# Performance work log

Measured on AMD Instinct MI355X. Metric: run time of the kernel, lower is better.

The kernel has to match this reference:

```python
import jax, jax.numpy as jnp
import numpy as np

NUM_HEADS = 16
HEAD_DIM = 64
HIDDEN = NUM_HEADS * HEAD_DIM


def _rope_tables(seq_len, dim, dtype):
    # inv_freq: [dim/2]; emb = cat(freqs, freqs): [S, dim]
    inv_freq = 1.0 / (10000.0 ** (jnp.arange(0, dim, 2, dtype=jnp.float32) / dim))
    t = jnp.arange(seq_len, dtype=jnp.float32)
    freqs = jnp.einsum('i,j->ij', t, inv_freq)
    emb = jnp.concatenate([freqs, freqs], axis=-1)
    return jnp.cos(emb).astype(dtype), jnp.sin(emb).astype(dtype)  # [S, dim] each


def _rotate_half(x):
    x1, x2 = jnp.split(x, 2, axis=-1)
    return jnp.concatenate([-x2, x1], axis=-1)


def setup_inputs() -> dict:
    key = jax.random.key(0)
    k1, k2, k3, k4 = jax.random.split(key, 4)
    B, S = 2, 2048
    hidden_states = jax.random.normal(k1, (B, S, HIDDEN), dtype=jnp.float32)
    scale = 0.02
    Wq = jax.random.normal(k2, (HIDDEN, HIDDEN), dtype=jnp.float32) * scale
    Wk = jax.random.normal(k3, (HIDDEN, HIDDEN), dtype=jnp.float32) * scale
    Wv = jax.random.normal(k4, (HIDDEN, HIDDEN), dtype=jnp.float32) * scale
    return {"hidden_states": hidden_states, "Wq": Wq, "Wk": Wk, "Wv": Wv}


def reference(hidden_states, Wq, Wk, Wv):
    B, S, H = hidden_states.shape
    # nn.Linear: x @ W.T ; reshape to [B, heads, S, head_dim]
    def split_heads(x):
        return x.reshape(B, S, NUM_HEADS, HEAD_DIM).transpose(0, 2, 1, 3)
    q = split_heads(hidden_states @ Wq.T)
    k = split_heads(hidden_states @ Wk.T)
    v = split_heads(hidden_states @ Wv.T)
    # inline RoPE over full head_dim
    cos, sin = _rope_tables(S, HEAD_DIM, q.dtype)  # [S, head_dim]
    cos = cos[None, None]  # [1,1,S,head_dim]
    sin = sin[None, None]
    q = q * cos + _rotate_half(q) * sin
    k = k * cos + _rotate_half(k) * sin
    # manual softmax attention
    scores = jnp.einsum('bhqd,bhkd->bhqk', q, k) / (HEAD_DIM ** 0.5)
    probs = jax.nn.softmax(scores, axis=-1)
    ctx = jnp.einsum('bhqk,bhkd->bhqd', probs, v)
    ctx = ctx.transpose(0, 2, 1, 3).reshape(B, S, H)
    return ctx
```

## Files before the change

### kernel.cpp

```cpp
#include <hip/hip_runtime.h>
#include <math.h>

#define NHEADS 16
#define HDIM   64
#define HID    1024
#define BATCH  2
#define SEQ    2048
#define NX (BATCH*SEQ*HID)
#define NW (HID*HID)

typedef unsigned short u16;
typedef __attribute__((ext_vector_type(8))) short  bf16x8;
typedef __attribute__((ext_vector_type(8))) unsigned short u16x8;
typedef __attribute__((ext_vector_type(4))) float  f32x4;


__device__ __forceinline__ void split8(const float* xf, bf16x8& hi, bf16x8& lo) {
#pragma unroll
    for (int j = 0; j < 8; j++) {
        unsigned u = __float_as_uint(xf[j]);
        hi[j] = (short)(u >> 16);
        float hf = __uint_as_float(u & 0xFFFF0000u);
        lo[j] = (short)(__float_as_uint(xf[j] - hf) >> 16);
    }
}
__device__ __forceinline__ void split1(float v, u16& h, u16& l) {
    unsigned u = __float_as_uint(v);
    h = (u16)(u >> 16);
    l = (u16)(__float_as_uint(v - __uint_as_float(u & 0xFFFF0000u)) >> 16);
}

__global__ void rope_tables_kernel(float* __restrict__ ct, float* __restrict__ st) {
    int idx = blockIdx.x * 256 + threadIdx.x;
    if (idx >= SEQ * HDIM) return;
    int s  = idx >> 6;
    int dh = idx & 63;
    int i  = dh & 31;
    float inv = exp2f(-(float)i * (13.28771237954945f / 32.0f));
    float fr  = (float)s * inv;
    ct[idx] = cosf(fr);
    st[idx] = sinf(fr);
}

__global__ void split_kernel(const float* __restrict__ X,
                             const float* __restrict__ W0,
                             const float* __restrict__ W1,
                             const float* __restrict__ W2,
                             u16* __restrict__ Xhi, u16* __restrict__ Xlo,
                             u16* __restrict__ Whi, u16* __restrict__ Wlo)
{
    long idx = ((long)blockIdx.x * 256 + threadIdx.x) * 4;
    if (idx >= (long)NX + 3L * NW) return;
    const float* src; u16* dh; u16* dl; long off;
    if (idx < NX) { src = X; dh = Xhi; dl = Xlo; off = idx; }
    else {
        long rr = idx - NX;
        int wi = (int)(rr >> 20);
        off = rr & (NW - 1);
        src = (wi == 0) ? W0 : ((wi == 1) ? W1 : W2);
        dh = Whi + (size_t)wi * NW;
        dl = Wlo + (size_t)wi * NW;
    }
    const int r = (int)(off >> 10);
    const int k = (int)(off & 1023);
    const size_t fo = ((size_t)(r >> 4) * 32 + (k >> 5)) * 512
                    + (size_t)((k >> 3) & 3) * 128 + (size_t)(r & 15) * 8 + (k & 7);
    float4 v = *(const float4*)(src + off);
    const float* vf = (const float*)&v;
    ushort4 h4, l4;
    u16* hp = (u16*)&h4; u16* lp = (u16*)&l4;
#pragma unroll
    for (int e = 0; e < 4; e++) split1(vf[e], hp[e], lp[e]);
    *(ushort4*)(dh + fo) = h4;
    *(ushort4*)(dl + fo) = l4;
}

__global__ __launch_bounds__(256, 2) void qkv_mfma_kernel(
    const u16* __restrict__ Xhi, const u16* __restrict__ Xlo,
    const u16* __restrict__ Whi, const u16* __restrict__ Wlo,
    const float* __restrict__ ct, const float* __restrict__ st,
    u16* __restrict__ Qhi, u16* __restrict__ Qlo,
    u16* __restrict__ Khi, u16* __restrict__ Klo,
    u16* __restrict__ Vhi, u16* __restrict__ Vlo)
{
    __shared__ unsigned vtr[64][129];

    const int t    = threadIdx.x;
    const int lane = t & 63;
    const int w    = t >> 6;
    const int lx   = lane & 15;
    const int quad = lane >> 4;
    const int proj = blockIdx.z;
    const int n0   = blockIdx.x * 128;
    const int m0   = blockIdx.y * 128;

    const u16* __restrict__ Wph = Whi + (size_t)proj * NW;
    const u16* __restrict__ Wpl = Wlo + (size_t)proj * NW;

    const int am = (w & 1) * 64;
    const int bn = (w >> 1) * 64;
    const int lp = quad * 128 + lx * 8;

    const u16 *pAh[4], *pAl[4], *pBh[4], *pBl[4];
#pragma unroll
    for (int i = 0; i < 4; i++) {
        const size_t o = ((size_t)(((m0 + am) >> 4) + i) * 32) * 512 + lp;
        pAh[i] = Xhi + o; pAl[i] = Xlo + o;
    }
#pragma unroll
    for (int j = 0; j < 4; j++) {
        const size_t o = ((size_t)(((n0 + bn) >> 4) + j) * 32) * 512 + lp;
        pBh[j] = Wph + o; pBl[j] = Wpl + o;
    }

    f32x4 acc[4][4];
#pragma unroll
    for (int i = 0; i < 4; i++)
#pragma unroll
        for (int j = 0; j < 4; j++) acc[i][j] = (f32x4){0.f, 0.f, 0.f, 0.f};

    bf16x8 cah[4], cal[4], cbh[4], cbl[4];
#pragma unroll
    for (int i = 0; i < 4; i++) { cah[i] = *(const bf16x8*)(pAh[i]); cal[i] = *(const bf16x8*)(pAl[i]); }
#pragma unroll
    for (int j = 0; j < 4; j++) { cbh[j] = *(const bf16x8*)(pBh[j]); cbl[j] = *(const bf16x8*)(pBl[j]); }

#pragma unroll 1
    for (int kt = 0; kt < HID; kt += 32) {
        const int ko = (kt + 32 < HID) ? ((kt + 32) >> 5) * 512 : 0;
        bf16x8 nah[4], nal[4], nbh[4], nbl[4];
#pragma unroll
        for (int i = 0; i < 4; i++) { nah[i] = *(const bf16x8*)(pAh[i] + ko); nal[i] = *(const bf16x8*)(pAl[i] + ko); }
#pragma unroll
        for (int j = 0; j < 4; j++) { nbh[j] = *(const bf16x8*)(pBh[j] + ko); nbl[j] = *(const bf16x8*)(pBl[j] + ko); }

#pragma unroll
        for (int j = 0; j < 4; j++)
#pragma unroll
            for (int i = 0; i < 4; i++) {
                acc[i][j] = __builtin_amdgcn_mfma_f32_16x16x32_bf16(cah[i], cbh[j], acc[i][j], 0, 0, 0);
                acc[i][j] = __builtin_amdgcn_mfma_f32_16x16x32_bf16(cal[i], cbh[j], acc[i][j], 0, 0, 0);
                acc[i][j] = __builtin_amdgcn_mfma_f32_16x16x32_bf16(cah[i], cbl[j], acc[i][j], 0, 0, 0);
            }
#pragma unroll
        for (int i = 0; i < 4; i++) { cah[i] = nah[i]; cal[i] = nal[i]; }
#pragma unroll
        for (int j = 0; j < 4; j++) { cbh[j] = nbh[j]; cbl[j] = nbl[j]; }
    }

    const int b      = m0 >> 11;
    const int head   = (n0 >> 6) + (w >> 1);
    const int m_base = m0 + am;

    if (proj < 2) {
#pragma unroll
        for (int i = 0; i < 4; i++) {
#pragma unroll
            for (int r = 0; r < 4; r++) {
                const int s = (m_base + i * 16 + quad * 4 + r) & 2047;
                const float* ctr = ct + s * HDIM;
                const float* str = st + s * HDIM;
                float nv[4];
#pragma unroll
                for (int j = 0; j < 4; j++) {
                    const int dh = j * 16 + lx;
                    const float c  = ctr[dh];
                    const float sn = str[dh];
                    const float x  = acc[i][j][r];
                    const float p  = acc[i][j ^ 2][r];
                    nv[j] = (j < 2) ? (x * c - p * sn) : (x * c + p * sn);
                }
#pragma unroll
                for (int j = 0; j < 4; j++) acc[i][j][r] = nv[j];
            }
        }
        u16* dh_ = (proj == 0) ? Qhi : Khi;
        u16* dl_ = (proj == 0) ? Qlo : Klo;
        const float qscale = (proj == 0) ? 0.18033688011112042f : 1.0f;
        const size_t obase = (size_t)(b * NHEADS + head) * SEQ * HDIM;
#pragma unroll
        for (int i = 0; i < 4; i++)
#pragma unroll
            for (int r = 0; r < 4; r++) {
                const int s   = (m_base + i * 16 + quad * 4 + r) & 2047;
                const int rb  = s >> 4;
                const int lxq = s & 15;
#pragma unroll
                for (int j = 0; j < 4; j++) {
                    const size_t fo = obase + ((size_t)rb * 2 + (j >> 1)) * 512
                                    + (size_t)((j & 1) * 2 + (lx >> 3)) * 128
                                    + (size_t)lxq * 8 + (lx & 7);
                    u16 hh, ll;
                    split1(acc[i][j][r] * qscale, hh, ll);
                    dh_[fo] = hh;
                    dl_[fo] = ll;
                }
            }
    } else {
#pragma unroll 1
        for (int pass = 0; pass < 2; pass++) {
            __syncthreads();
            if ((w & 1) == pass) {
#pragma unroll
                for (int i = 0; i < 4; i++)
#pragma unroll
                    for (int j = 0; j < 4; j++)
#pragma unroll
                        for (int r = 0; r < 4; r++) {
                            const int ml = i * 16 + quad * 4 + r;
                            const int nl = bn + j * 16 + lx;
                            const float v = acc[i][j][r];
                            unsigned u  = __float_as_uint(v);
                            unsigned hi = u & 0xFFFF0000u;
                            unsigned lo = __float_as_uint(v - __uint_as_float(hi)) >> 16;
                            vtr[ml][nl] = hi | lo;
                        }
            }
            __syncthreads();
            {
                const int d      = t >> 1;
                const int sh     = (t & 1) * 32;
                const int headv  = (n0 >> 6) + (d >> 6);
                const int dd     = d & 63;
                const size_t vbase = (size_t)(b * NHEADS + headv) * SEQ * HDIM;
                const int s0base = (m0 & 2047) + pass * 64 + sh;
#pragma unroll
                for (int k = 0; k < 4; k++) {
                    const int s0 = s0base + k * 8;
                    u16x8 hv, lv;
#pragma unroll
                    for (int e = 0; e < 8; e++) {
                        unsigned u = vtr[sh + k * 8 + e][d];
                        hv[e] = (u16)(u >> 16);
                        lv[e] = (u16)(u & 0xFFFFu);
                    }
                    const size_t fo = vbase + ((size_t)(dd >> 4) * 64 + (s0 >> 5)) * 512
                                    + (size_t)((s0 >> 3) & 3) * 128 + (size_t)(dd & 15) * 8;
                    *(u16x8*)(Vhi + fo) = hv;
                    *(u16x8*)(Vlo + fo) = lv;
                }
            }
        }
    }
}

__global__ __launch_bounds__(256, 2) void attn_kernel(
    const u16* __restrict__ Qhi, const u16* __restrict__ Qlo,
    const u16* __restrict__ Khi, const u16* __restrict__ Klo,
    const u16* __restrict__ Vhi, const u16* __restrict__ Vlo,
    float* __restrict__ OUT)
{
    __shared__ float PS[4][32][68];

    const int t    = threadIdx.x;
    const int lane = t & 63;
    const int w    = t >> 6;
    const int lx   = lane & 15;
    const int quad = lane >> 4;

    const int q0 = blockIdx.x * 128;
    const int h  = blockIdx.y;
    const int b  = blockIdx.z;
    const size_t base = (size_t)(b * NHEADS + h) * SEQ * HDIM;
    const int lp = quad * 128 + lx * 8;

    bf16x8 qh[2][2], ql[2][2];
#pragma unroll
    for (int a = 0; a < 2; a++)
#pragma unroll
        for (int ks = 0; ks < 2; ks++) {
            const size_t fo = base + ((size_t)((q0 >> 4) + w * 2 + a) * 2 + ks) * 512 + lp;
            qh[a][ks] = *(const bf16x8*)(Qhi + fo);
            ql[a][ks] = *(const bf16x8*)(Qlo + fo);
        }

    f32x4 O[2][4];
    float l_part[2][4];
#pragma unroll
    for (int a = 0; a < 2; a++) {
#pragma unroll
        for (int dt = 0; dt < 4; dt++) O[a][dt] = (f32x4){0.f,0.f,0.f,0.f};
#pragma unroll
        for (int r = 0; r < 4; r++) l_part[a][r] = 0.f;
    }

    bf16x8 kAh[2][4], kAl[2][4], kBh[2][4], kBl[2][4];
#pragma unroll
    for (int c = 0; c < 4; c++)
#pragma unroll
        for (int ks = 0; ks < 2; ks++) {
            const size_t fo = base + ((size_t)c * 2 + ks) * 512 + lp;
            kAh[ks][c] = *(const bf16x8*)(Khi + fo);
            kAl[ks][c] = *(const bf16x8*)(Klo + fo);
        }

    auto tile_body = [&](bf16x8 (&ckh)[2][4], bf16x8 (&ckl)[2][4],
                         bf16x8 (&nkh)[2][4], bf16x8 (&nkl)[2][4],
                         int kt, int ktn) {
        bf16x8 vh[2][4], vl[2][4];
#pragma unroll
        for (int dt = 0; dt < 4; dt++)
#pragma unroll
            for (int ks2 = 0; ks2 < 2; ks2++) {
                const size_t fo = base + ((size_t)dt * 64 + (kt >> 5) + ks2) * 512 + lp;
                vh[ks2][dt] = *(const bf16x8*)(Vhi + fo);
                vl[ks2][dt] = *(const bf16x8*)(Vlo + fo);
            }

#pragma unroll
        for (int a = 0; a < 2; a++) {
#pragma unroll
            for (int c = 0; c < 4; c++) {
                f32x4 acc = (f32x4){0.f,0.f,0.f,0.f};
#pragma unroll
                for (int ks = 0; ks < 2; ks++) {
                    acc = __builtin_amdgcn_mfma_f32_16x16x32_bf16(qh[a][ks], ckh[ks][c], acc, 0, 0, 0);
                    acc = __builtin_amdgcn_mfma_f32_16x16x32_bf16(ql[a][ks], ckh[ks][c], acc, 0, 0, 0);
                    acc = __builtin_amdgcn_mfma_f32_16x16x32_bf16(qh[a][ks], ckl[ks][c], acc, 0, 0, 0);
                }
#pragma unroll
                for (int r = 0; r < 4; r++) {
                    float p = exp2f(acc[r]);
                    l_part[a][r] += p;
                    PS[w][a * 16 + quad * 4 + r][c * 16 + lx] = p;
                }
            }
        }

#pragma unroll
        for (int c = 0; c < 4; c++)
#pragma unroll
            for (int ks = 0; ks < 2; ks++) {
                const size_t fo = base + ((size_t)((ktn >> 4) + c) * 2 + ks) * 512 + lp;
                nkh[ks][c] = *(const bf16x8*)(Khi + fo);
                nkl[ks][c] = *(const bf16x8*)(Klo + fo);
            }

#pragma unroll
        for (int a = 0; a < 2; a++) {
#pragma unroll
            for (int ks2 = 0; ks2 < 2; ks2++) {
                const float* ps = &PS[w][a * 16 + lx][ks2 * 32 + quad * 8];
                float pf[8];
                *(float4*)&pf[0] = *(const float4*)ps;
                *(float4*)&pf[4] = *(const float4*)(ps + 4);
                bf16x8 phi, plo;
                split8(pf, phi, plo);
#pragma unroll
                for (int dt = 0; dt < 4; dt++) {
                    O[a][dt] = __builtin_amdgcn_mfma_f32_16x16x32_bf16(phi, vh[ks2][dt], O[a][dt], 0, 0, 0);
                    O[a][dt] = __builtin_amdgcn_mfma_f32_16x16x32_bf16(plo, vh[ks2][dt], O[a][dt], 0, 0, 0);
                    O[a][dt] = __builtin_amdgcn_mfma_f32_16x16x32_bf16(phi, vl[ks2][dt], O[a][dt], 0, 0, 0);
                }
            }
        }
    };

#pragma unroll 1
    for (int kt = 0; kt < SEQ; kt += 128) {
        tile_body(kAh, kAl, kBh, kBl, kt,       kt + 64);
        tile_body(kBh, kBl, kAh, kAl, kt + 64, (kt + 128) & (SEQ - 1));
    }

    float linv[2][4];
#pragma unroll
    for (int a = 0; a < 2; a++)
#pragma unroll
        for (int r = 0; r < 4; r++) {
            float l = l_part[a][r];
            l += __shfl_xor(l, 1);
            l += __shfl_xor(l, 2);
            l += __shfl_xor(l, 4);
            l += __shfl_xor(l, 8);
            linv[a][r] = 1.f / l;
        }

    float* Po = &PS[0][0][0];
    __syncthreads();
#pragma unroll
    for (int a = 0; a < 2; a++)
#pragma unroll
        for (int dt = 0; dt < 4; dt++)
#pragma unroll
            for (int r = 0; r < 4; r++)
                Po[(size_t)(w * 32 + a * 16 + quad * 4 + r) * 68 + dt * 16 + lx] =
                    O[a][dt][r] * linv[a][r];
    __syncthreads();
    {
        const int q    = t >> 1;
        const int half = t & 1;
        const float* prow = Po + (size_t)q * 68 + half * 32;
        float* dst = OUT + ((size_t)(b * SEQ + q0 + q)) * HID + h * HDIM + half * 32;
#pragma unroll
        for (int e = 0; e < 8; e++)
            ((float4*)dst)[e] = ((const float4*)prow)[e];
    }
}

extern "C" void kernel_launch(void* const* d_in, const int* in_sizes, int n_in,
                              void* d_out, int out_size, void* d_ws, size_t ws_size,
                              hipStream_t stream)
{
    const float* X  = (const float*)d_in[0];
    const float* Wq = (const float*)d_in[1];
    const float* Wk = (const float*)d_in[2];
    const float* Wv = (const float*)d_in[3];
    float* out = (float*)d_out;

    const size_t qkv_elems = (size_t)BATCH * NHEADS * SEQ * HDIM;
    char* wsb = (char*)d_ws;
    float* ct  = (float*)wsb;
    float* st  = ct + (size_t)SEQ * HDIM;
    u16* Xhi = (u16*)(st + (size_t)SEQ * HDIM);
    u16* Xlo = Xhi + (size_t)NX;
    u16* Whi = Xlo + (size_t)NX;
    u16* Wlo = Whi + 3 * (size_t)NW;
    u16* Qhi = Wlo + 3 * (size_t)NW;
    u16* Qlo = Qhi + qkv_elems;
    u16* Khi = Qlo + qkv_elems;
    u16* Klo = Khi + qkv_elems;
    u16* Vhi = Klo + qkv_elems;
    u16* Vlo = Vhi + qkv_elems;

    rope_tables_kernel<<<(SEQ * HDIM + 255) / 256, 256, 0, stream>>>(ct, st);

    const long tot = (long)NX + 3L * NW;
    split_kernel<<<(int)((tot / 4 + 255) / 256), 256, 0, stream>>>(
        X, Wq, Wk, Wv, Xhi, Xlo, Whi, Wlo);

    qkv_mfma_kernel<<<dim3(HID / 128, (BATCH * SEQ) / 128, 3), 256, 0, stream>>>(
        Xhi, Xlo, Whi, Wlo, ct, st, Qhi, Qlo, Khi, Klo, Vhi, Vlo);

    attn_kernel<<<dim3(SEQ / 128, NHEADS, BATCH), 256, 0, stream>>>(
        Qhi, Qlo, Khi, Klo, Vhi, Vlo, out);
}
```

Before: 309.6 us.

## Split attention KV range across two blocks and add combine kernel

Each attention block now handles half of the key/value sequence for its 128 queries, doubling the grid. Blocks write unnormalized partial outputs and row sums to workspace. A new combine kernel adds the two halves and normalizes into the final layout. The aim is more parallelism and better CU utilization, at the cost of extra global traffic for the partials and one more kernel launch.

```diff
diff --git a/kernel.cpp b/kernel.cpp
--- a/kernel.cpp
+++ b/kernel.cpp
@@ -248,9 +248,10 @@
     const u16* __restrict__ Qhi, const u16* __restrict__ Qlo,
     const u16* __restrict__ Khi, const u16* __restrict__ Klo,
     const u16* __restrict__ Vhi, const u16* __restrict__ Vlo,
-    float* __restrict__ OUT)
+    float* __restrict__ OP, float* __restrict__ LP)
 {
     __shared__ float PS[4][32][68];
+    __shared__ float lsh[128];
 
     const int t    = threadIdx.x;
     const int lane = t & 63;
@@ -258,7 +259,9 @@
     const int lx   = lane & 15;
     const int quad = lane >> 4;
 
-    const int q0 = blockIdx.x * 128;
+    const int q0  = (blockIdx.x >> 1) * 128;
+    const int kvh = blockIdx.x & 1;
+    const int kt0 = kvh * (SEQ / 2);
     const int h  = blockIdx.y;
     const int b  = blockIdx.z;
     const size_t base = (size_t)(b * NHEADS + h) * SEQ * HDIM;
@@ -289,7 +292,7 @@
     for (int c = 0; c < 4; c++)
 #pragma unroll
         for (int ks = 0; ks < 2; ks++) {
-            const size_t fo = base + ((size_t)c * 2 + ks) * 512 + lp;
+            const size_t fo = base + ((size_t)((kt0 >> 4) + c) * 2 + ks) * 512 + lp;
             kAh[ks][c] = *(const bf16x8*)(Khi + fo);
             kAl[ks][c] = *(const bf16x8*)(Klo + fo);
         }
@@ -357,12 +360,12 @@
     };
 
 #pragma unroll 1
-    for (int kt = 0; kt < SEQ; kt += 128) {
-        tile_body(kAh, kAl, kBh, kBl, kt,       kt + 64);
-        tile_body(kBh, kBl, kAh, kAl, kt + 64, (kt + 128) & (SEQ - 1));
-    }
-
-    float linv[2][4];
+    for (int kt = kt0; kt < kt0 + SEQ / 2; kt += 128) {
+        tile_body(kAh, kAl, kBh, kBl, kt,      kt + 64);
+        tile_body(kBh, kBl, kAh, kAl, kt + 64, kt0 + ((kt + 128 - kt0) & (SEQ / 2 - 1)));
+    }
+
+    float lred[2][4];
 #pragma unroll
     for (int a = 0; a < 2; a++)
 #pragma unroll
@@ -372,29 +375,58 @@
             l += __shfl_xor(l, 2);
             l += __shfl_xor(l, 4);
             l += __shfl_xor(l, 8);
-            linv[a][r] = 1.f / l;
+            lred[a][r] = l;
         }
 
     float* Po = &PS[0][0][0];
     __syncthreads();
 #pragma unroll
-    for (int a = 0; a < 2; a++)
+    for (int a = 0; a < 2; a++) {
 #pragma unroll
         for (int dt = 0; dt < 4; dt++)
 #pragma unroll
             for (int r = 0; r < 4; r++)
                 Po[(size_t)(w * 32 + a * 16 + quad * 4 + r) * 68 + dt * 16 + lx] =
-                    O[a][dt][r] * linv[a][r];
+                    O[a][dt][r];
+#pragma unroll
+        for (int r = 0; r < 4; r++)
+            if (lx == 0) lsh[w * 32 + a * 16 + quad * 4 + r] = lred[a][r];
+    }
     __syncthreads();
     {
+        const size_t pbase = ((size_t)((kvh * BATCH + b) * NHEADS + h) * SEQ + q0);
         const int q    = t >> 1;
         const int half = t & 1;
         const float* prow = Po + (size_t)q * 68 + half * 32;
-        float* dst = OUT + ((size_t)(b * SEQ + q0 + q)) * HID + h * HDIM + half * 32;
+        float* dst = OP + (pbase + q) * HDIM + half * 32;
 #pragma unroll
         for (int e = 0; e < 8; e++)
             ((float4*)dst)[e] = ((const float4*)prow)[e];
-    }
+        if (t < 128) LP[pbase + t] = lsh[t];
+    }
+}
+
+__global__ __launch_bounds__(256) void combine_kernel(
+    const float* __restrict__ OP, const float* __restrict__ LP,
+    float* __restrict__ OUT)
+{
+    const int idx = blockIdx.x * 256 + threadIdx.x;
+    const int d4 = idx & 15;
+    const int h  = (idx >> 4) & 15;
+    const int s  = (idx >> 8) & (SEQ - 1);
+    const int b  = idx >> 19;
+    const size_t half_stride = (size_t)BATCH * NHEADS * SEQ;
+    const size_t li = (size_t)(b * NHEADS + h) * SEQ + s;
+    const size_t o0 = li * HDIM + d4 * 4;
+    const float4 v0 = *(const float4*)(OP + o0);
+    const float4 v1 = *(const float4*)(OP + o0 + half_stride * HDIM);
+    const float inv = 1.f / (LP[li] + LP[li + half_stride]);
+    float4 o;
+    o.x = (v0.x + v1.x) * inv;
+    o.y = (v0.y + v1.y) * inv;
+    o.z = (v0.z + v1.z) * inv;
+    o.w = (v0.w + v1.w) * inv;
+    *(float4*)(OUT + ((size_t)(b * SEQ + s)) * HID + h * HDIM + d4 * 4) = o;
 }
 
 extern "C" void kernel_launch(void* const* d_in, const int* in_sizes, int n_in,
@@ -421,6 +453,8 @@
     u16* Klo = Khi + qkv_elems;
     u16* Vhi = Klo + qkv_elems;
     u16* Vlo = Vhi + qkv_elems;
+    float* OP = (float*)(Vlo + qkv_elems);
+    float* LP = OP + 2 * qkv_elems;
 
     rope_tables_kernel<<<(SEQ * HDIM + 255) / 256, 256, 0, stream>>>(ct, st);
 
@@ -431,6 +465,9 @@
     qkv_mfma_kernel<<<dim3(HID / 128, (BATCH * SEQ) / 128, 3), 256, 0, stream>>>(
         Xhi, Xlo, Whi, Wlo, ct, st, Qhi, Qlo, Khi, Klo, Vhi, Vlo);
 
-    attn_kernel<<<dim3(SEQ / 128, NHEADS, BATCH), 256, 0, stream>>>(
-        Qhi, Qlo, Khi, Klo, Vhi, Vlo, out);
-}
+    attn_kernel<<<dim3((SEQ / 128) * 2, NHEADS, BATCH), 256, 0, stream>>>(
+        Qhi, Qlo, Khi, Klo, Vhi, Vlo, OP, LP);
+
+    combine_kernel<<<(BATCH * SEQ * NHEADS * 16) / 256, 256, 0, stream>>>(
+        OP, LP, out);
+}
```

Result: slower. 388.6 us (+25.5%).
